# Performance work log

Hardware: AMD Instinct MI355X
Metric: run time of the kernel (lower is better)

The kernel has to match this reference:

```python
import jax, jax.numpy as jnp
import numpy as np

MIN_RANGE = -128.0
MAX_RANGE = 127.0


def quantize(t, min_range=MIN_RANGE, max_range=MAX_RANGE):
    """Per-tensor affine (asymmetric) quantization, as in QuantizedMatrix.
    Returns (q, scale, zero_point) with q in [min_range, max_range]."""
    mn = jnp.min(t)
    mx = jnp.max(t)
    scale = (mx - mn) / (max_range - min_range)
    zero_point = jnp.round(min_range - mn / scale)
    q = jnp.clip(jnp.round(t / scale) + zero_point, min_range, max_range)
    return q, scale, zero_point


def setup_inputs() -> dict:
    key = jax.random.key(0)
    k1, k2, k3 = jax.random.split(key, 3)
    B, S, D_IN, D_OUT = 4, 2048, 4096, 4096
    x = jax.random.normal(k1, (B, S, D_IN), dtype=jnp.float32)
    # nn.Linear weight layout: [out_features, in_features]
    W = jax.random.normal(k2, (D_OUT, D_IN), dtype=jnp.float32) * (1.0 / np.sqrt(D_IN))
    bias = jax.random.normal(k3, (D_OUT,), dtype=jnp.float32) * 0.02
    return {"x": x, "W": W, "bias": bias}


def reference(x, W, bias):
    # Quantize activations (per-tensor over the whole [B,S,D] tensor) and weights.
    qx, sx, zx = quantize(x)
    qw, sw, zw = quantize(W)
    # QuantizedMatrix matmul: dequantized product
    #   s_x * s_w * (q_x - z_x) @ (q_w - z_w)^T  , W is [out,in] so contract on 'd'.
    acc = jnp.einsum("bsd,od->bso", qx - zx, qw - zw)
    res = (sx * sw) * acc + bias
    return res
```

## Files before the change

### kernel.cpp

```cpp
#include <hip/hip_runtime.h>
#include <hip/hip_bf16.h>

#define GM 8192
#define GN 4096
#define GK 4096

#define QX_OFF   0ull
#define QW_OFF   33554432ull
#define RSX_OFF  50331648ull
#define RSW_OFF  50364416ull
#define ATOM_OFF 50380800ull
#define PRM_OFF  50380832ull

using v4i  = __attribute__((ext_vector_type(4)))  int;
using v16i = __attribute__((ext_vector_type(16))) int;

__device__ __forceinline__ unsigned encf(float x) {
    unsigned u = __float_as_uint(x);
    return (u & 0x80000000u) ? ~u : (u | 0x80000000u);
}
__device__ __forceinline__ float decf(unsigned e) {
    unsigned u = (e & 0x80000000u) ? (e & 0x7FFFFFFFu) : ~e;
    return __uint_as_float(u);
}

__device__ __forceinline__ void async16(const signed char* g, signed char* l) {
    __builtin_amdgcn_global_load_lds((const __attribute__((address_space(1))) void*)g,
                                     (__attribute__((address_space(3))) void*)l,
                                     16, 0, 0);
}

__global__ void k_init(unsigned* slots) {
    if (threadIdx.x < 4) slots[threadIdx.x] = 0u;
}

__global__ void k_minmax(const float4* __restrict__ x, const float4* __restrict__ Wt,
                         unsigned* slots) {
    const float4* p; int n4, b0, nb; unsigned* sl;
    if (blockIdx.x < 4096) { p = x;  n4 = GM * GK / 4; b0 = blockIdx.x;        nb = 4096; sl = slots;     }
    else                   { p = Wt; n4 = GN * GK / 4; b0 = blockIdx.x - 4096; nb = 2048; sl = slots + 2; }
    unsigned mx = 0u, nm = 0u;
    for (int i = b0 * 256 + threadIdx.x; i < n4; i += nb * 256) {
        float4 v = p[i];
        mx = max(mx, encf(v.x)); nm = max(nm, encf(-v.x));
        mx = max(mx, encf(v.y)); nm = max(nm, encf(-v.y));
        mx = max(mx, encf(v.z)); nm = max(nm, encf(-v.z));
        mx = max(mx, encf(v.w)); nm = max(nm, encf(-v.w));
    }
    #pragma unroll
    for (int o = 32; o > 0; o >>= 1) {
        mx = max(mx, (unsigned)__shfl_down((int)mx, o));
        nm = max(nm, (unsigned)__shfl_down((int)nm, o));
    }
    __shared__ unsigned smx[4], snm[4];
    int w = threadIdx.x >> 6;
    if ((threadIdx.x & 63) == 0) { smx[w] = mx; snm[w] = nm; }
    __syncthreads();
    if (threadIdx.x == 0) {
        #pragma unroll
        for (int i = 1; i < 4; i++) { mx = max(mx, smx[i]); nm = max(nm, snm[i]); }
        atomicMax(&sl[0], mx);
        atomicMax(&sl[1], nm);
    }
}

__global__ void k_params(const unsigned* __restrict__ slots, float* prm) {
    if (threadIdx.x == 0) {
        float mxx = decf(slots[0]), mnx = -decf(slots[1]);
        float sx  = (mxx - mnx) / 255.0f;
        float zxf = rintf(-128.0f - mnx / sx);
        float mxw = decf(slots[2]), mnw = -decf(slots[3]);
        float sw  = (mxw - mnw) / 255.0f;
        float zwf = rintf(-128.0f - mnw / sw);
        prm[0] = sx; prm[1] = zxf; prm[2] = sw; prm[3] = zwf; prm[4] = sx * sw;
        int* ip = (int*)prm;
        ip[5] = (int)zxf; ip[6] = (int)zwf;
    }
}

__global__ void k_quant(const float* __restrict__ x, const float* __restrict__ Wt,
                        signed char* __restrict__ qx, signed char* __restrict__ qw,
                        int* __restrict__ rsx, int* __restrict__ rsw,
                        const float* __restrict__ prm) {
    const float* src; signed char* q; int* rs; int pidx, row;
    if (blockIdx.x < GM) { row = blockIdx.x;      src = x;  q = qx; rs = rsx; pidx = 0; }
    else                 { row = blockIdx.x - GM; src = Wt; q = qw; rs = rsw; pidx = 2; }
    const int t = threadIdx.x;
    const float s  = prm[pidx];
    const float zp = prm[pidx + 1];
    const float4* srow = (const float4*)(src + (size_t)row * GK);
    int* qrow = (int*)(q + (size_t)row * GK);
    int acc = 0;
    #pragma unroll
    for (int i = 0; i < 4; i++) {
        float4 v = srow[i * 256 + t];
        int q0 = (int)fminf(fmaxf(rintf(v.x / s) + zp, -128.0f), 127.0f);
        int q1 = (int)fminf(fmaxf(rintf(v.y / s) + zp, -128.0f), 127.0f);
        int q2 = (int)fminf(fmaxf(rintf(v.z / s) + zp, -128.0f), 127.0f);
        int q3 = (int)fminf(fmaxf(rintf(v.w / s) + zp, -128.0f), 127.0f);
        acc += q0 + q1 + q2 + q3;
        qrow[i * 256 + t] = (q0 & 255) | ((q1 & 255) << 8) | ((q2 & 255) << 16)
                          | ((q3 & 255) << 24);
    }
    #pragma unroll
    for (int o = 32; o > 0; o >>= 1) acc += __shfl_down(acc, o);
    __shared__ int sa[4];
    if ((t & 63) == 0) sa[t >> 6] = acc;
    __syncthreads();
    if (t == 0) rs[row] = sa[0] + sa[1] + sa[2] + sa[3];
}

__global__ __launch_bounds__(512, 2) void k_gemm(
    const signed char* __restrict__ qx, const signed char* __restrict__ qw,
    const int* __restrict__ rsx, const int* __restrict__ rsw,
    const float* __restrict__ bias, const float* __restrict__ prm,
    float* __restrict__ out) {
    __shared__ __align__(16) signed char lds[2][2][256 * 64];

    const int tid  = threadIdx.x;
    const int lane = tid & 63;
    const int w    = tid >> 6;
    const int bid  = blockIdx.x;
    const int tm0  = (bid >> 4) * 256;
    const int tn0  = (bid & 15) * 256;

    const int slab = w & 3;
    const int sr   = lane >> 2;
    const int sc   = ((lane & 3) ^ (sr & 3)) * 16;
    const signed char* gsrc = (w < 4)
        ? qx + (size_t)(tm0 + slab * 64 + sr) * GK + sc
        : qw + (size_t)(tn0 + slab * 64 + sr) * GK + sc;
    const int ldsTensor = (w < 4) ? 0 : 1;
    const int ldsSlab   = slab * 64 * 64;

    const int wr = w >> 2;
    const int wc = w & 3;
    const int fr = lane & 31;
    const int fh = lane >> 5;

    v16i acc[4][2] = {};

    #pragma unroll
    for (int j = 0; j < 4; j++)
        async16(gsrc + (size_t)j * 16 * GK,
                &lds[0][ldsTensor][ldsSlab + j * 1024]);
    __syncthreads();

    for (int kt = 0; kt < GK / 64; ++kt) {
        const int cur = kt & 1;
        if (kt + 1 < GK / 64) {
            const size_t ko = (size_t)(kt + 1) * 64;
            #pragma unroll
            for (int j = 0; j < 4; j++)
                async16(gsrc + (size_t)j * 16 * GK + ko,
                        &lds[cur ^ 1][ldsTensor][ldsSlab + j * 1024]);
        }
        const signed char* cA = lds[cur][0];
        const signed char* cB = lds[cur][1];
        #pragma unroll
        for (int s = 0; s < 2; s++) {
            const int cc = s * 2 + fh;
            const int ca = (cc ^ (fr & 3)) * 16;
            v4i a0 = *(const v4i*)(cA + (wr * 128      + fr) * 64 + ca);
            v4i a1 = *(const v4i*)(cA + (wr * 128 + 32 + fr) * 64 + ca);
            v4i a2 = *(const v4i*)(cA + (wr * 128 + 64 + fr) * 64 + ca);
            v4i a3 = *(const v4i*)(cA + (wr * 128 + 96 + fr) * 64 + ca);
            v4i b0 = *(const v4i*)(cB + (wc * 64       + fr) * 64 + ca);
            v4i b1 = *(const v4i*)(cB + (wc * 64  + 32 + fr) * 64 + ca);
            acc[0][0] = __builtin_amdgcn_mfma_i32_32x32x32_i8(a0, b0, acc[0][0], 0, 0, 0);
            acc[0][1] = __builtin_amdgcn_mfma_i32_32x32x32_i8(a0, b1, acc[0][1], 0, 0, 0);
            acc[1][0] = __builtin_amdgcn_mfma_i32_32x32x32_i8(a1, b0, acc[1][0], 0, 0, 0);
            acc[1][1] = __builtin_amdgcn_mfma_i32_32x32x32_i8(a1, b1, acc[1][1], 0, 0, 0);
            acc[2][0] = __builtin_amdgcn_mfma_i32_32x32x32_i8(a2, b0, acc[2][0], 0, 0, 0);
            acc[2][1] = __builtin_amdgcn_mfma_i32_32x32x32_i8(a2, b1, acc[2][1], 0, 0, 0);
            acc[3][0] = __builtin_amdgcn_mfma_i32_32x32x32_i8(a3, b0, acc[3][0], 0, 0, 0);
            acc[3][1] = __builtin_amdgcn_mfma_i32_32x32x32_i8(a3, b1, acc[3][1], 0, 0, 0);
        }
        __syncthreads();
    }

    const float sxsw = prm[4];
    const int* ip = (const int*)prm;
    const int zxi = ip[5], zwi = ip[6];
    const int kzz = GK * zxi * zwi;
    #pragma unroll
    for (int i = 0; i < 4; i++) {
        #pragma unroll
        for (int j = 0; j < 2; j++) {
            const int col = tn0 + wc * 64 + j * 32 + fr;
            const int ccol = kzz - zxi * rsw[col];
            const float bv = bias[col];
            #pragma unroll
            for (int reg = 0; reg < 16; reg++) {
                const int row = tm0 + wr * 128 + i * 32
                              + (reg & 3) + 8 * (reg >> 2) + 4 * fh;
                const int t = acc[i][j][reg] - zwi * rsx[row] + ccol;
                out[(size_t)row * GN + col] = fmaf(sxsw, (float)t, bv);
            }
        }
    }
}

extern "C" void kernel_launch(void* const* d_in, const int* in_sizes, int n_in,
                              void* d_out, int out_size, void* d_ws, size_t ws_size,
                              hipStream_t stream) {
    const float* x    = (const float*)d_in[0];
    const float* Wt   = (const float*)d_in[1];
    const float* bias = (const float*)d_in[2];
    float* out = (float*)d_out;

    char* ws = (char*)d_ws;
    signed char* qx = (signed char*)(ws + QX_OFF);
    signed char* qw = (signed char*)(ws + QW_OFF);
    int* rsx = (int*)(ws + RSX_OFF);
    int* rsw = (int*)(ws + RSW_OFF);
    unsigned* slots = (unsigned*)(ws + ATOM_OFF);
    float* prm = (float*)(ws + PRM_OFF);

    k_init<<<1, 64, 0, stream>>>(slots);
    k_minmax<<<6144, 256, 0, stream>>>((const float4*)x, (const float4*)Wt, slots);
    k_params<<<1, 1, 0, stream>>>(slots, prm);
    k_quant<<<GM + GN, 256, 0, stream>>>(x, Wt, qx, qw, rsx, rsw, prm);
    k_gemm<<<(GM / 256) * (GN / 256), 512, 0, stream>>>(qx, qw, rsx, rsw, bias,
                                                        prm, out);
}
```

Baseline: 532.5 us.

## Triple-buffer GEMM LDS pipeline, retune swizzle, replace atomic min/max with partials

The GEMM main loop moves from a double-buffered LDS scheme with a full __syncthreads per tile to a three-stage ring. It uses explicit s_waitcnt vmcnt and a raw barrier, so two tile loads stay in flight while the current tile is computed. The LDS XOR swizzle is changed on both the load and read sides to reduce bank conflicts. The min/max reduction drops the init kernel and global atomics: each block writes a partial, and a 256-thread params kernel reduces them, with fewer minmax blocks. The extra LDS buffer (96KB per block) may reduce occupancy below the declared two blocks per CU.

```diff
diff --git a/kernel.cpp b/kernel.cpp
--- a/kernel.cpp
+++ b/kernel.cpp
@@ -1,16 +1,18 @@
 #include <hip/hip_runtime.h>
-#include <hip/hip_bf16.h>
 
 #define GM 8192
 #define GN 4096
 #define GK 4096
+#define NT (GK / 64)
 
 #define QX_OFF   0ull
 #define QW_OFF   33554432ull
 #define RSX_OFF  50331648ull
 #define RSW_OFF  50364416ull
-#define ATOM_OFF 50380800ull
 #define PRM_OFF  50380832ull
+
+#define MMB_X 2048
+#define MMB_W 1024
 
 using v4i  = __attribute__((ext_vector_type(4)))  int;
 using v16i = __attribute__((ext_vector_type(16))) int;
@@ -30,15 +32,11 @@
                                      16, 0, 0);
 }
 
-__global__ void k_init(unsigned* slots) {
-    if (threadIdx.x < 4) slots[threadIdx.x] = 0u;
-}
-
 __global__ void k_minmax(const float4* __restrict__ x, const float4* __restrict__ Wt,
-                         unsigned* slots) {
-    const float4* p; int n4, b0, nb; unsigned* sl;
-    if (blockIdx.x < 4096) { p = x;  n4 = GM * GK / 4; b0 = blockIdx.x;        nb = 4096; sl = slots;     }
-    else                   { p = Wt; n4 = GN * GK / 4; b0 = blockIdx.x - 4096; nb = 2048; sl = slots + 2; }
+                         unsigned* __restrict__ part) {
+    const float4* p; int n4, b0, nb; unsigned* dst;
+    if (blockIdx.x < MMB_X) { p = x;  n4 = GM * GK / 4; b0 = blockIdx.x;         nb = MMB_X; dst = part;        }
+    else                    { p = Wt; n4 = GN * GK / 4; b0 = blockIdx.x - MMB_X; nb = MMB_W; dst = part + 4096; }
     unsigned mx = 0u, nm = 0u;
     for (int i = b0 * 256 + threadIdx.x; i < n4; i += nb * 256) {
         float4 v = p[i];
@@ -59,17 +57,43 @@
     if (threadIdx.x == 0) {
         #pragma unroll
         for (int i = 1; i < 4; i++) { mx = max(mx, smx[i]); nm = max(nm, snm[i]); }
-        atomicMax(&sl[0], mx);
-        atomicMax(&sl[1], nm);
-    }
-}
-
-__global__ void k_params(const unsigned* __restrict__ slots, float* prm) {
-    if (threadIdx.x == 0) {
-        float mxx = decf(slots[0]), mnx = -decf(slots[1]);
+        dst[b0]      = mx;
+        dst[nb + b0] = nm;
+    }
+}
+
+__global__ void k_params(const unsigned* __restrict__ part, float* prm) {
+    const int t = threadIdx.x;
+    unsigned v0 = 0u, v1 = 0u, v2 = 0u, v3 = 0u;
+    for (int i = t; i < MMB_X; i += 256) {
+        v0 = max(v0, part[i]);
+        v1 = max(v1, part[MMB_X + i]);
+    }
+    for (int i = t; i < MMB_W; i += 256) {
+        v2 = max(v2, part[4096 + i]);
+        v3 = max(v3, part[5120 + i]);
+    }
+    #pragma unroll
+    for (int o = 32; o > 0; o >>= 1) {
+        v0 = max(v0, (unsigned)__shfl_down((int)v0, o));
+        v1 = max(v1, (unsigned)__shfl_down((int)v1, o));
+        v2 = max(v2, (unsigned)__shfl_down((int)v2, o));
+        v3 = max(v3, (unsigned)__shfl_down((int)v3, o));
+    }
+    __shared__ unsigned s[4][4];
+    const int wv = t >> 6;
+    if ((t & 63) == 0) { s[wv][0] = v0; s[wv][1] = v1; s[wv][2] = v2; s[wv][3] = v3; }
+    __syncthreads();
+    if (t == 0) {
+        #pragma unroll
+        for (int i = 1; i < 4; i++) {
+            v0 = max(v0, s[i][0]); v1 = max(v1, s[i][1]);
+            v2 = max(v2, s[i][2]); v3 = max(v3, s[i][3]);
+        }
+        float mxx = decf(v0), mnx = -decf(v1);
         float sx  = (mxx - mnx) / 255.0f;
         float zxf = rintf(-128.0f - mnx / sx);
-        float mxw = decf(slots[2]), mnw = -decf(slots[3]);
+        float mxw = decf(v2), mnw = -decf(v3);
         float sw  = (mxw - mnw) / 255.0f;
         float zwf = rintf(-128.0f - mnw / sw);
         prm[0] = sx; prm[1] = zxf; prm[2] = sw; prm[3] = zwf; prm[4] = sx * sw;
@@ -115,7 +139,7 @@
     const int* __restrict__ rsx, const int* __restrict__ rsw,
     const float* __restrict__ bias, const float* __restrict__ prm,
     float* __restrict__ out) {
-    __shared__ __align__(16) signed char lds[2][2][256 * 64];
+    __shared__ __align__(16) signed char lds[3][2][256 * 64];
 
     const int tid  = threadIdx.x;
     const int lane = tid & 63;
@@ -126,7 +150,7 @@
 
     const int slab = w & 3;
     const int sr   = lane >> 2;
-    const int sc   = ((lane & 3) ^ (sr & 3)) * 16;
+    const int sc   = ((lane & 3) ^ ((lane >> 3) & 3)) * 16;
     const signed char* gsrc = (w < 4)
         ? qx + (size_t)(tm0 + slab * 64 + sr) * GK + sc
         : qw + (size_t)(tn0 + slab * 64 + sr) * GK + sc;
@@ -140,27 +164,13 @@
 
     v16i acc[4][2] = {};
 
-    #pragma unroll
-    for (int j = 0; j < 4; j++)
-        async16(gsrc + (size_t)j * 16 * GK,
-                &lds[0][ldsTensor][ldsSlab + j * 1024]);
-    __syncthreads();
-
-    for (int kt = 0; kt < GK / 64; ++kt) {
-        const int cur = kt & 1;
-        if (kt + 1 < GK / 64) {
-            const size_t ko = (size_t)(kt + 1) * 64;
-            #pragma unroll
-            for (int j = 0; j < 4; j++)
-                async16(gsrc + (size_t)j * 16 * GK + ko,
-                        &lds[cur ^ 1][ldsTensor][ldsSlab + j * 1024]);
-        }
-        const signed char* cA = lds[cur][0];
-        const signed char* cB = lds[cur][1];
+    auto compute = [&](int rdi) {
+        const signed char* cA = lds[rdi][0];
+        const signed char* cB = lds[rdi][1];
         #pragma unroll
         for (int s = 0; s < 2; s++) {
             const int cc = s * 2 + fh;
-            const int ca = (cc ^ (fr & 3)) * 16;
+            const int ca = (cc ^ ((fr >> 1) & 3)) * 16;
             v4i a0 = *(const v4i*)(cA + (wr * 128      + fr) * 64 + ca);
             v4i a1 = *(const v4i*)(cA + (wr * 128 + 32 + fr) * 64 + ca);
             v4i a2 = *(const v4i*)(cA + (wr * 128 + 64 + fr) * 64 + ca);
@@ -176,8 +186,38 @@
             acc[3][0] = __builtin_amdgcn_mfma_i32_32x32x32_i8(a3, b0, acc[3][0], 0, 0, 0);
             acc[3][1] = __builtin_amdgcn_mfma_i32_32x32x32_i8(a3, b1, acc[3][1], 0, 0, 0);
         }
-        __syncthreads();
-    }
+    };
+
+    #pragma unroll
+    for (int j = 0; j < 4; j++)
+        async16(gsrc + (size_t)j * 16 * GK, &lds[0][ldsTensor][ldsSlab + j * 1024]);
+    #pragma unroll
+    for (int j = 0; j < 4; j++)
+        async16(gsrc + (size_t)j * 16 * GK + 64, &lds[1][ldsTensor][ldsSlab + j * 1024]);
+
+    int rd = 0;
+    for (int kt = 0; kt < NT - 2; ++kt) {
+        asm volatile("s_waitcnt vmcnt(4)" ::: "memory");
+        __builtin_amdgcn_s_barrier();
+        asm volatile("" ::: "memory");
+        int st = rd + 2; if (st >= 3) st -= 3;
+        const size_t ko = (size_t)(kt + 2) * 64;
+        #pragma unroll
+        for (int j = 0; j < 4; j++)
+            async16(gsrc + (size_t)j * 16 * GK + ko,
+                    &lds[st][ldsTensor][ldsSlab + j * 1024]);
+        compute(rd);
+        rd = (rd + 1 == 3) ? 0 : rd + 1;
+    }
+    asm volatile("s_waitcnt vmcnt(4)" ::: "memory");
+    __builtin_amdgcn_s_barrier();
+    asm volatile("" ::: "memory");
+    compute(rd);
+    rd = (rd + 1 == 3) ? 0 : rd + 1;
+    asm volatile("s_waitcnt vmcnt(0)" ::: "memory");
+    __builtin_amdgcn_s_barrier();
+    asm volatile("" ::: "memory");
+    compute(rd);
 
     const float sxsw = prm[4];
     const int* ip = (const int*)prm;
@@ -214,12 +254,11 @@
     signed char* qw = (signed char*)(ws + QW_OFF);
     int* rsx = (int*)(ws + RSX_OFF);
     int* rsw = (int*)(ws + RSW_OFF);
-    unsigned* slots = (unsigned*)(ws + ATOM_OFF);
+    unsigned* part = (unsigned*)(ws + QX_OFF);
     float* prm = (float*)(ws + PRM_OFF);
 
-    k_init<<<1, 64, 0, stream>>>(slots);
-    k_minmax<<<6144, 256, 0, stream>>>((const float4*)x, (const float4*)Wt, slots);
-    k_params<<<1, 1, 0, stream>>>(slots, prm);
+    k_minmax<<<MMB_X + MMB_W, 256, 0, stream>>>((const float4*)x, (const float4*)Wt, part);
+    k_params<<<1, 256, 0, stream>>>(part, prm);
     k_quant<<<GM + GN, 256, 0, stream>>>(x, Wt, qx, qw, rsx, rsw, prm);
     k_gemm<<<(GM / 256) * (GN / 256), 512, 0, stream>>>(qx, qw, rsx, rsw, bias,
                                                         prm, out);
```

New measurement: 440.7 us. -17.2%, faster.
